# Optimization experiments

Measured on AMD Instinct MI355X. Metric: run time of the kernel, lower is better.

Reference implementation:

```python
import jax, jax.numpy as jnp
import numpy as np

DIM = 256
HEADS = 4
HID = 64
GROUPS = 32
HHD = HEADS * HID  # 256
EPS = 1e-5


def group_norm(x, gamma, beta):
    # x: (B, C, H, W)
    B, C, H, W = x.shape
    xg = x.reshape(B, GROUPS, C // GROUPS, H, W)
    mean = xg.mean(axis=(2, 3, 4), keepdims=True)
    var = xg.var(axis=(2, 3, 4), keepdims=True)
    xg = (xg - mean) * jax.lax.rsqrt(var + EPS)
    xn = xg.reshape(B, C, H, W)
    return xn * gamma[None, :, None, None] + beta[None, :, None, None]


def conv1x1(x, w, b):
    # x: (B, Cin, H, W), w: (Cout, Cin), b: (Cout,)
    return jnp.einsum('bchw,oc->bohw', x, w) + b[None, :, None, None]


def setup_inputs() -> dict:
    key = jax.random.key(0)
    ks = jax.random.split(key, 9)
    x = jax.random.normal(ks[0], (64, DIM, 32, 32), dtype=jnp.float32)
    s_in = 1.0 / np.sqrt(DIM)
    s_out = 1.0 / np.sqrt(HHD)
    wq = jax.random.uniform(ks[1], (HHD, DIM), jnp.float32, -s_in, s_in)
    bq = jax.random.uniform(ks[2], (HHD,), jnp.float32, -s_in, s_in)
    wk = jax.random.uniform(ks[3], (HHD, DIM), jnp.float32, -s_in, s_in)
    bk = jax.random.uniform(ks[4], (HHD,), jnp.float32, -s_in, s_in)
    wv = jax.random.uniform(ks[5], (HHD, DIM), jnp.float32, -s_in, s_in)
    bv = jax.random.uniform(ks[6], (HHD,), jnp.float32, -s_in, s_in)
    wo = jax.random.uniform(ks[7], (DIM, HHD), jnp.float32, -s_out, s_out)
    bo = jax.random.uniform(ks[8], (DIM,), jnp.float32, -s_out, s_out)
    gamma = jnp.ones((DIM,), jnp.float32)
    beta = jnp.zeros((DIM,), jnp.float32)
    return {"x": x, "wq": wq, "bq": bq, "wk": wk, "bk": bk, "wv": wv,
            "bv": bv, "wo": wo, "bo": bo, "gamma": gamma, "beta": beta}


def reference(x, wq, bq, wk, bk, wv, bv, wo, bo, gamma, beta):
    B, C, H, W = x.shape
    xn = group_norm(x, gamma, beta)  # residual uses normalized x (as in source)
    q = conv1x1(xn, wq, bq)  # (B, HHD, H, W)
    k = conv1x1(xn, wk, bk)
    v = conv1x1(xn, wv, bv)
    hw = H * W
    q = q.transpose(0, 2, 3, 1).reshape(B, hw, HHD)   # (B, HW, C)
    k = k.reshape(B, HHD, hw)                          # (B, C, HW)
    v = v.transpose(0, 2, 3, 1).reshape(B, hw, HHD)
    scale = 1.0 / np.sqrt(HID)  # source scales by sqrt(hidden_dimension) only
    qk = jnp.einsum('bnc,bcm->bnm', q, k) * scale      # (B, HW, HW)
    attn = jax.nn.softmax(qk, axis=-1)
    out = jnp.einsum('bnm,bmc->bnc', attn, v)          # (B, HW, HHD)
    out = out.reshape(B, H, W, HHD).transpose(0, 3, 1, 2)
    out = conv1x1(out, wo, bo)                         # (B, DIM, H, W)
    return xn + out
```

## Files before the change

### kernel.cpp

```cpp
#include <hip/hip_runtime.h>
#include <hip/hip_bf16.h>

typedef __attribute__((ext_vector_type(8))) short short8;
typedef __attribute__((ext_vector_type(4))) float f32x4;
typedef __attribute__((ext_vector_type(4))) unsigned short us4;

#define MFMA16(a,b,c) __builtin_amdgcn_mfma_f32_16x16x32_bf16((a),(b),(c),0,0,0)

__device__ __forceinline__ unsigned short f2bf(float x){
  union{float f; unsigned u;} v; v.f=x;
  unsigned r = v.u + 0x7fffu + ((v.u>>16)&1u);
  return (unsigned short)(r>>16);
}
__device__ __forceinline__ float bf2f(unsigned short u){
  union{unsigned u; float f;} v; v.u = ((unsigned)u)<<16; return v.f;
}

__global__ __launch_bounds__(256) void prep_kernel(
    const float* __restrict__ wq, const float* __restrict__ wk,
    const float* __restrict__ wv, const float* __restrict__ wo,
    unsigned short* __restrict__ dst){
  int idx = (blockIdx.x*256 + threadIdx.x)*4;
  const float* srcs[4] = {wq, wk, wv, wo};
  int m = idx >> 16;
  float4 v = *(const float4*)(srcs[m] + (idx & 65535));
  us4 o; o[0]=f2bf(v.x); o[1]=f2bf(v.y); o[2]=f2bf(v.z); o[3]=f2bf(v.w);
  *(us4*)(dst + idx) = o;
}

__global__ __launch_bounds__(256) void gn_kernel(
    const float* __restrict__ x, const float* __restrict__ gamma,
    const float* __restrict__ beta,
    unsigned short* __restrict__ xn_cm, unsigned short* __restrict__ xn_pm){
  int b = blockIdx.x >> 5, g = blockIdx.x & 31;
  int t = threadIdx.x;
  const float* xb = x + (size_t)(b*256 + g*8)*1024;
  float4 v[8]; float s=0.f, ss=0.f;
  #pragma unroll
  for(int j=0;j<8;++j){
    v[j] = ((const float4*)xb)[j*256 + t];
    s  += v[j].x+v[j].y+v[j].z+v[j].w;
    ss += v[j].x*v[j].x+v[j].y*v[j].y+v[j].z*v[j].z+v[j].w*v[j].w;
  }
  #pragma unroll
  for(int m=1;m<64;m<<=1){ s += __shfl_xor(s,m); ss += __shfl_xor(ss,m); }
  __shared__ float red[8];
  if((t&63)==0){ red[t>>6]=s; red[4+(t>>6)]=ss; }
  __syncthreads();
  s  = red[0]+red[1]+red[2]+red[3];
  ss = red[4]+red[5]+red[6]+red[7];
  float mean = s*(1.f/8192.f);
  float rstd = rsqrtf(ss*(1.f/8192.f) - mean*mean + 1e-5f);
  float fn[8][4];
  #pragma unroll
  for(int j=0;j<8;++j){
    float ga = gamma[g*8+j]*rstd;
    float be = beta[g*8+j] - mean*ga;
    fn[j][0]=v[j].x*ga+be; fn[j][1]=v[j].y*ga+be;
    fn[j][2]=v[j].z*ga+be; fn[j][3]=v[j].w*ga+be;
    us4 o; o[0]=f2bf(fn[j][0]); o[1]=f2bf(fn[j][1]);
          o[2]=f2bf(fn[j][2]); o[3]=f2bf(fn[j][3]);
    *(us4*)(xn_cm + (size_t)(b*256 + g*8 + j)*1024 + 4*t) = o;
  }
  #pragma unroll
  for(int pp=0;pp<4;++pp){
    short8 w8;
    #pragma unroll
    for(int j=0;j<8;++j) w8[j] = (short)f2bf(fn[j][pp]);
    *(short8*)(xn_pm + (size_t)(b*1024 + 4*t + pp)*256 + g*8) = w8;
  }
}

__global__ __launch_bounds__(256) void qkv_kernel(
    const unsigned short* __restrict__ xn_pm, const unsigned short* __restrict__ wbf,
    const float* __restrict__ bq, const float* __restrict__ bk,
    const float* __restrict__ bv,
    unsigned short* __restrict__ qb, unsigned short* __restrict__ kb,
    unsigned short* __restrict__ vTb){
  int b = blockIdx.y, z = blockIdx.z;
  int otile = blockIdx.x & 3, ptile = blockIdx.x >> 2;
  int t = threadIdx.x, w = t>>6, lane = t&63, lo = lane&15, hi = lane>>4;
  const unsigned short* W = wbf + (size_t)z*65536;
  const float* bias = (z==0)? bq : ((z==1)? bk : bv);
  const unsigned short* xb = xn_pm + (size_t)b*1024*256;
  int p0 = ptile*256 + w*64;
  f32x4 acc[4][4] = {};
  if(z < 2){
    #pragma unroll
    for(int kk=0;kk<8;++kk){
      short8 af[4], bfr[4];
      #pragma unroll
      for(int r=0;r<4;++r)
        af[r] = *(const short8*)(W + (size_t)(otile*64 + r*16 + lo)*256 + kk*32 + hi*8);
      #pragma unroll
      for(int c=0;c<4;++c)
        bfr[c] = *(const short8*)(xb + (size_t)(p0 + c*16 + lo)*256 + kk*32 + hi*8);
      #pragma unroll
      for(int r=0;r<4;++r)
        #pragma unroll
        for(int c=0;c<4;++c) acc[r][c] = MFMA16(af[r], bfr[c], acc[r][c]);
    }
    unsigned short* dst = (z==0)? qb : kb;
    float scale = (z==0)? 0.125f : 1.0f;
    #pragma unroll
    for(int r=0;r<4;++r){
      int ob = otile*64 + r*16 + hi*4;
      float4 bi = *(const float4*)(bias + ob);
      float bia[4] = {bi.x, bi.y, bi.z, bi.w};
      #pragma unroll
      for(int c=0;c<4;++c){
        int p = p0 + c*16 + lo;
        us4 stv;
        #pragma unroll
        for(int rg=0; rg<4; ++rg) stv[rg] = f2bf((acc[r][c][rg] + bia[rg])*scale);
        *(us4*)(dst + (size_t)(b*1024 + p)*256 + ob) = stv;
      }
    }
  } else {
    #pragma unroll
    for(int kk=0;kk<8;++kk){
      short8 af[4], bfr[4];
      #pragma unroll
      for(int r=0;r<4;++r)
        af[r] = *(const short8*)(xb + (size_t)(p0 + r*16 + lo)*256 + kk*32 + hi*8);
      #pragma unroll
      for(int c=0;c<4;++c)
        bfr[c] = *(const short8*)(W + (size_t)(otile*64 + c*16 + lo)*256 + kk*32 + hi*8);
      #pragma unroll
      for(int r=0;r<4;++r)
        #pragma unroll
        for(int c=0;c<4;++c) acc[r][c] = MFMA16(af[r], bfr[c], acc[r][c]);
    }
    #pragma unroll
    for(int c=0;c<4;++c){
      int o = otile*64 + c*16 + lo;
      float bia = bias[o];
      #pragma unroll
      for(int r=0;r<4;++r){
        int pb = p0 + r*16 + hi*4;
        us4 stv;
        #pragma unroll
        for(int rg=0; rg<4; ++rg) stv[rg] = f2bf(acc[r][c][rg] + bia);
        *(us4*)(vTb + (size_t)b*262144 + (size_t)o*1024 + pb) = stv;
      }
    }
  }
}

__global__ __launch_bounds__(256) void attn_kernel(
    const unsigned short* __restrict__ qb, const unsigned short* __restrict__ kb,
    const unsigned short* __restrict__ vT, const unsigned short* __restrict__ wo_bf,
    const float* __restrict__ bo, const unsigned short* __restrict__ xn_cm,
    float* __restrict__ out){
  int qt = blockIdx.x, b = blockIdx.y;
  int t = threadIdx.x, w = t>>6, lane = t&63, lo = lane&15, hi = lane>>4;
  __shared__ unsigned short smem_u[21248];
  unsigned short* k_lds = smem_u;
  unsigned short* v_lds = smem_u + 8448;
  unsigned short* p_lds = smem_u + 18688 + w*640;
  unsigned short* o_lds = smem_u + w*4224;

  short8 aq[8];
  const unsigned short* qrow = qb + (size_t)(b*1024 + qt*64 + w*16 + lo)*256;
  #pragma unroll
  for(int kk=0;kk<8;++kk) aq[kk] = *(const short8*)(qrow + kk*32 + hi*8);

  f32x4 oc[16] = {};
  float mr[4] = {-1e30f,-1e30f,-1e30f,-1e30f};
  float lr[4] = {0.f,0.f,0.f,0.f};

  const unsigned short* kbase = kb + (size_t)b*1024*256;
  const unsigned short* vbase = vT + (size_t)b*256*1024;

  for(int kv0=0; kv0<1024; kv0+=32){
    __syncthreads();
    {
      const short8* src = (const short8*)(kbase + (size_t)kv0*256);
      #pragma unroll
      for(int i=0;i<4;++i){
        int u = i*256 + t;
        *(short8*)(k_lds + (u>>5)*264 + (u&31)*8) = src[u];
      }
      #pragma unroll
      for(int i=0;i<4;++i){
        int u = i*256 + t;
        int c = u>>2, part = u&3;
        *(short8*)(v_lds + c*40 + part*8) =
            *(const short8*)(vbase + (size_t)c*1024 + kv0 + part*8);
      }
    }
    __syncthreads();
    f32x4 sc[2] = {};
    #pragma unroll
    for(int kk=0;kk<8;++kk){
      short8 b0 = *(const short8*)(k_lds + lo*264      + kk*32 + hi*8);
      short8 b1 = *(const short8*)(k_lds + (16+lo)*264 + kk*32 + hi*8);
      sc[0] = MFMA16(aq[kk], b0, sc[0]);
      sc[1] = MFMA16(aq[kk], b1, sc[1]);
    }
    float pr[2][4];
    #pragma unroll
    for(int r=0;r<4;++r){
      float tm = fmaxf(sc[0][r], sc[1][r]);
      tm = fmaxf(tm, __shfl_xor(tm,1)); tm = fmaxf(tm, __shfl_xor(tm,2));
      tm = fmaxf(tm, __shfl_xor(tm,4)); tm = fmaxf(tm, __shfl_xor(tm,8));
      float mnew  = fmaxf(mr[r], tm);
      float alpha = __expf(mr[r]-mnew);
      mr[r] = mnew;
      float p0v = __expf(sc[0][r]-mnew);
      float p1v = __expf(sc[1][r]-mnew);
      pr[0][r]=p0v; pr[1][r]=p1v;
      float rs = p0v + p1v;
      rs += __shfl_xor(rs,1); rs += __shfl_xor(rs,2);
      rs += __shfl_xor(rs,4); rs += __shfl_xor(rs,8);
      lr[r] = lr[r]*alpha + rs;
      #pragma unroll
      for(int f=0; f<16; ++f) oc[f][r] *= alpha;
    }
    #pragma unroll
    for(int cf=0;cf<2;++cf)
      #pragma unroll
      for(int r=0;r<4;++r)
        p_lds[(hi*4+r)*40 + cf*16 + lo] = f2bf(pr[cf][r]);
    short8 pa = *(const short8*)(p_lds + lo*40 + hi*8);
    #pragma unroll
    for(int f=0; f<16; ++f){
      short8 bv = *(const short8*)(v_lds + (f*16+lo)*40 + hi*8);
      oc[f] = MFMA16(pa, bv, oc[f]);
    }
  }

  float inv[4];
  #pragma unroll
  for(int r=0;r<4;++r) inv[r] = 1.f/lr[r];
  __syncthreads();
  #pragma unroll
  for(int f=0;f<16;++f)
    #pragma unroll
    for(int r=0;r<4;++r)
      o_lds[(hi*4+r)*264 + f*16 + lo] = f2bf(oc[f][r]*inv[r]);

  f32x4 a2[16] = {};
  #pragma unroll
  for(int kk=0;kk<8;++kk){
    short8 pa2 = *(const short8*)(o_lds + lo*264 + kk*32 + hi*8);
    #pragma unroll
    for(int cf=0;cf<16;++cf){
      short8 wb = *(const short8*)(wo_bf + (size_t)(cf*16+lo)*256 + kk*32 + hi*8);
      a2[cf] = MFMA16(pa2, wb, a2[cf]);
    }
  }
  int p0 = qt*64 + w*16 + hi*4;
  #pragma unroll
  for(int cf=0;cf<16;++cf){
    int o = cf*16 + lo;
    float bia = bo[o];
    us4 xr = *(const us4*)(xn_cm + (size_t)(b*256+o)*1024 + p0);
    float4 st;
    st.x = a2[cf][0] + bia + bf2f(xr[0]);
    st.y = a2[cf][1] + bia + bf2f(xr[1]);
    st.z = a2[cf][2] + bia + bf2f(xr[2]);
    st.w = a2[cf][3] + bia + bf2f(xr[3]);
    *(float4*)(out + (size_t)(b*256+o)*1024 + p0) = st;
  }
}

extern "C" void kernel_launch(void* const* d_in, const int* in_sizes, int n_in,
                              void* d_out, int out_size, void* d_ws, size_t ws_size,
                              hipStream_t stream){
  (void)in_sizes; (void)n_in; (void)out_size; (void)ws_size;
  const float* x     = (const float*)d_in[0];
  const float* wq    = (const float*)d_in[1];
  const float* bq    = (const float*)d_in[2];
  const float* wk    = (const float*)d_in[3];
  const float* bk    = (const float*)d_in[4];
  const float* wv    = (const float*)d_in[5];
  const float* bv    = (const float*)d_in[6];
  const float* wo    = (const float*)d_in[7];
  const float* bo    = (const float*)d_in[8];
  const float* gamma = (const float*)d_in[9];
  const float* beta  = (const float*)d_in[10];
  float* out = (float*)d_out;
  char* ws = (char*)d_ws;
  unsigned short* xn_cm = (unsigned short*)(ws);
  unsigned short* xn_pm = (unsigned short*)(ws + 33554432);
  unsigned short* qb    = (unsigned short*)(ws + 67108864);
  unsigned short* kb    = (unsigned short*)(ws + 100663296);
  unsigned short* vT    = (unsigned short*)(ws + 134217728);
  unsigned short* wbf   = (unsigned short*)(ws + 167772160);

  hipLaunchKernelGGL(prep_kernel, dim3(256), dim3(256), 0, stream, wq, wk, wv, wo, wbf);
  hipLaunchKernelGGL(gn_kernel,   dim3(2048), dim3(256), 0, stream, x, gamma, beta, xn_cm, xn_pm);
  hipLaunchKernelGGL(qkv_kernel,  dim3(16,64,3), dim3(256), 0, stream,
                     xn_pm, wbf, bq, bk, bv, qb, kb, vT);
  hipLaunchKernelGGL(attn_kernel, dim3(16,64), dim3(256), 0, stream,
                     qb, kb, vT, wbf + 3*65536, bo, xn_cm, out);
}
```

Baseline: 613.4 us.

## Double-buffer K/V via global_load_lds with swizzled LDS and lazy softmax rescale

```diff
diff --git a/kernel.cpp b/kernel.cpp
--- a/kernel.cpp
+++ b/kernel.cpp
@@ -6,6 +6,9 @@
 typedef __attribute__((ext_vector_type(4))) unsigned short us4;
 
 #define MFMA16(a,b,c) __builtin_amdgcn_mfma_f32_16x16x32_bf16((a),(b),(c),0,0,0)
+#define GLOAD16(g,l) __builtin_amdgcn_global_load_lds( \
+    (const __attribute__((address_space(1))) void*)(g), \
+    (__attribute__((address_space(3))) void*)(l), 16, 0, 0)
 
 __device__ __forceinline__ unsigned short f2bf(float x){
   union{float f; unsigned u;} v; v.f=x;
@@ -147,93 +150,126 @@
   }
 }
 
-__global__ __launch_bounds__(256) void attn_kernel(
+__global__ __launch_bounds__(512, 4) void attn_kernel(
     const unsigned short* __restrict__ qb, const unsigned short* __restrict__ kb,
     const unsigned short* __restrict__ vT, const unsigned short* __restrict__ wo_bf,
     const float* __restrict__ bo, const unsigned short* __restrict__ xn_cm,
     float* __restrict__ out){
-  int qt = blockIdx.x, b = blockIdx.y;
+  int flat = blockIdx.x;
+  int xcd = flat & 7, rest = flat >> 3;
+  int b = xcd*8 + (rest>>3), qt = rest & 7;
   int t = threadIdx.x, w = t>>6, lane = t&63, lo = lane&15, hi = lane>>4;
-  __shared__ unsigned short smem_u[21248];
-  unsigned short* k_lds = smem_u;
-  unsigned short* v_lds = smem_u + 8448;
-  unsigned short* p_lds = smem_u + 18688 + w*640;
-  unsigned short* o_lds = smem_u + w*4224;
+
+  __shared__ unsigned short smem_u[37888];
+  unsigned short* kb0 = smem_u;
+  unsigned short* kb1 = smem_u + 8192;
+  unsigned short* vb0 = smem_u + 16384;
+  unsigned short* vb1 = smem_u + 24576;
+  unsigned short* p_lds = smem_u + 32768 + w*640;
+
+  const unsigned short* kbase = kb + (size_t)b*262144;
+  const unsigned short* vbase = vT + (size_t)b*262144;
+
+  int ku0 = w*128 + lane, ku1 = w*128 + 64 + lane;
+  int kr0 = ku0>>5, kr1 = ku1>>5;
+  int ksrc0 = kr0*256 + ((ku0&31)^(kr0&7))*8;
+  int ksrc1 = kr1*256 + ((ku1&31)^(kr1&7))*8;
+  int vc0 = ku0>>2, vc1 = ku1>>2;
+  int vsrc0 = vc0*1024 + ((ku0&3)^(vc0&3))*8;
+  int vsrc1 = vc1*1024 + ((ku1&3)^(vc1&3))*8;
+  int ldsA = (w*128)*8, ldsB = (w*128+64)*8;
+
+  int hxl8 = (hi ^ (lo&7))*8;
+  int vroff = lo*32 + (hi^(lo&3))*8;
 
   short8 aq[8];
-  const unsigned short* qrow = qb + (size_t)(b*1024 + qt*64 + w*16 + lo)*256;
-  #pragma unroll
-  for(int kk=0;kk<8;++kk) aq[kk] = *(const short8*)(qrow + kk*32 + hi*8);
-
+  {
+    const unsigned short* qrow = qb + (size_t)(b*1024 + qt*128 + w*16 + lo)*256 + hi*8;
+    #pragma unroll
+    for(int kk=0;kk<8;++kk) aq[kk] = *(const short8*)(qrow + kk*32);
+  }
   f32x4 oc[16] = {};
   float mr[4] = {-1e30f,-1e30f,-1e30f,-1e30f};
   float lr[4] = {0.f,0.f,0.f,0.f};
 
-  const unsigned short* kbase = kb + (size_t)b*1024*256;
-  const unsigned short* vbase = vT + (size_t)b*256*1024;
-
-  for(int kv0=0; kv0<1024; kv0+=32){
+  {
+    const unsigned short* kg = kbase;
+    const unsigned short* vg = vbase;
+    GLOAD16(kg + ksrc0, kb0 + 0 + ldsA);  GLOAD16(kg + ksrc1, kb0 + 0 + ldsB);
+    GLOAD16(vg + vsrc0, vb0 + 0 + ldsA);  GLOAD16(vg + vsrc1, vb0 + 0 + ldsB);
+  }
+  __syncthreads();
+
+  for(int tkv=0; tkv<32; ++tkv){
+    int cur = tkv & 1;
+    unsigned short* kc = cur ? kb1 : kb0;
+    unsigned short* vc = cur ? vb1 : vb0;
+    if(tkv < 31){
+      unsigned short* kn = cur ? kb0 : kb1;
+      unsigned short* vn = cur ? vb0 : vb1;
+      const unsigned short* kg = kbase + (tkv+1)*32*256;
+      const unsigned short* vg = vbase + (tkv+1)*32;
+      GLOAD16(kg + ksrc0, kn + ldsA);  GLOAD16(kg + ksrc1, kn + ldsB);
+      GLOAD16(vg + vsrc0, vn + ldsA);  GLOAD16(vg + vsrc1, vn + ldsB);
+    }
+    f32x4 sc0 = {}, sc1 = {};
+    __builtin_amdgcn_s_setprio(1);
+    #pragma unroll
+    for(int kk=0;kk<8;++kk){
+      int coff = (kk*32) ^ hxl8;
+      short8 b0 = *(const short8*)(kc + lo*256        + coff);
+      short8 b1 = *(const short8*)(kc + lo*256 + 4096 + coff);
+      sc0 = MFMA16(aq[kk], b0, sc0);
+      sc1 = MFMA16(aq[kk], b1, sc1);
+    }
+    __builtin_amdgcn_s_setprio(0);
+    float tm[4];
+    #pragma unroll
+    for(int r=0;r<4;++r){
+      float m2 = fmaxf(sc0[r], sc1[r]);
+      m2 = fmaxf(m2, __shfl_xor(m2,1)); m2 = fmaxf(m2, __shfl_xor(m2,2));
+      m2 = fmaxf(m2, __shfl_xor(m2,4)); m2 = fmaxf(m2, __shfl_xor(m2,8));
+      tm[r] = m2;
+    }
+    if(__any((tm[0]>mr[0]+8.f)|(tm[1]>mr[1]+8.f)|(tm[2]>mr[2]+8.f)|(tm[3]>mr[3]+8.f))){
+      #pragma unroll
+      for(int r=0;r<4;++r){
+        float mnew  = fmaxf(mr[r], tm[r]);
+        float alpha = __expf(mr[r]-mnew);
+        mr[r] = mnew; lr[r] *= alpha;
+        #pragma unroll
+        for(int f=0; f<16; ++f) oc[f][r] *= alpha;
+      }
+    }
+    #pragma unroll
+    for(int r=0;r<4;++r){
+      float p0 = __expf(sc0[r]-mr[r]);
+      float p1 = __expf(sc1[r]-mr[r]);
+      lr[r] += p0 + p1;
+      p_lds[(hi*4+r)*40 + lo]    = f2bf(p0);
+      p_lds[(hi*4+r)*40 + 16+lo] = f2bf(p1);
+    }
+    short8 pa = *(const short8*)(p_lds + lo*40 + hi*8);
+    __builtin_amdgcn_s_setprio(1);
+    #pragma unroll
+    for(int f=0; f<16; ++f){
+      short8 bv = *(const short8*)(vc + f*512 + vroff);
+      oc[f] = MFMA16(pa, bv, oc[f]);
+    }
+    __builtin_amdgcn_s_setprio(0);
     __syncthreads();
-    {
-      const short8* src = (const short8*)(kbase + (size_t)kv0*256);
-      #pragma unroll
-      for(int i=0;i<4;++i){
-        int u = i*256 + t;
-        *(short8*)(k_lds + (u>>5)*264 + (u&31)*8) = src[u];
-      }
-      #pragma unroll
-      for(int i=0;i<4;++i){
-        int u = i*256 + t;
-        int c = u>>2, part = u&3;
-        *(short8*)(v_lds + c*40 + part*8) =
-            *(const short8*)(vbase + (size_t)c*1024 + kv0 + part*8);
-      }
-    }
-    __syncthreads();
-    f32x4 sc[2] = {};
-    #pragma unroll
-    for(int kk=0;kk<8;++kk){
-      short8 b0 = *(const short8*)(k_lds + lo*264      + kk*32 + hi*8);
-      short8 b1 = *(const short8*)(k_lds + (16+lo)*264 + kk*32 + hi*8);
-      sc[0] = MFMA16(aq[kk], b0, sc[0]);
-      sc[1] = MFMA16(aq[kk], b1, sc[1]);
-    }
-    float pr[2][4];
-    #pragma unroll
-    for(int r=0;r<4;++r){
-      float tm = fmaxf(sc[0][r], sc[1][r]);
-      tm = fmaxf(tm, __shfl_xor(tm,1)); tm = fmaxf(tm, __shfl_xor(tm,2));
-      tm = fmaxf(tm, __shfl_xor(tm,4)); tm = fmaxf(tm, __shfl_xor(tm,8));
-      float mnew  = fmaxf(mr[r], tm);
-      float alpha = __expf(mr[r]-mnew);
-      mr[r] = mnew;
-      float p0v = __expf(sc[0][r]-mnew);
-      float p1v = __expf(sc[1][r]-mnew);
-      pr[0][r]=p0v; pr[1][r]=p1v;
-      float rs = p0v + p1v;
-      rs += __shfl_xor(rs,1); rs += __shfl_xor(rs,2);
-      rs += __shfl_xor(rs,4); rs += __shfl_xor(rs,8);
-      lr[r] = lr[r]*alpha + rs;
-      #pragma unroll
-      for(int f=0; f<16; ++f) oc[f][r] *= alpha;
-    }
-    #pragma unroll
-    for(int cf=0;cf<2;++cf)
-      #pragma unroll
-      for(int r=0;r<4;++r)
-        p_lds[(hi*4+r)*40 + cf*16 + lo] = f2bf(pr[cf][r]);
-    short8 pa = *(const short8*)(p_lds + lo*40 + hi*8);
-    #pragma unroll
-    for(int f=0; f<16; ++f){
-      short8 bv = *(const short8*)(v_lds + (f*16+lo)*40 + hi*8);
-      oc[f] = MFMA16(pa, bv, oc[f]);
-    }
-  }
-
+  }
+
+  #pragma unroll
+  for(int r=0;r<4;++r){
+    lr[r] += __shfl_xor(lr[r],1); lr[r] += __shfl_xor(lr[r],2);
+    lr[r] += __shfl_xor(lr[r],4); lr[r] += __shfl_xor(lr[r],8);
+  }
   float inv[4];
   #pragma unroll
   for(int r=0;r<4;++r) inv[r] = 1.f/lr[r];
-  __syncthreads();
+
+  unsigned short* o_lds = smem_u + w*4224;
   #pragma unroll
   for(int f=0;f<16;++f)
     #pragma unroll
@@ -250,18 +286,18 @@
       a2[cf] = MFMA16(pa2, wb, a2[cf]);
     }
   }
-  int p0 = qt*64 + w*16 + hi*4;
+  int p0r = qt*128 + w*16 + hi*4;
   #pragma unroll
   for(int cf=0;cf<16;++cf){
     int o = cf*16 + lo;
     float bia = bo[o];
-    us4 xr = *(const us4*)(xn_cm + (size_t)(b*256+o)*1024 + p0);
+    us4 xr = *(const us4*)(xn_cm + (size_t)(b*256+o)*1024 + p0r);
     float4 st;
     st.x = a2[cf][0] + bia + bf2f(xr[0]);
     st.y = a2[cf][1] + bia + bf2f(xr[1]);
     st.z = a2[cf][2] + bia + bf2f(xr[2]);
     st.w = a2[cf][3] + bia + bf2f(xr[3]);
-    *(float4*)(out + (size_t)(b*256+o)*1024 + p0) = st;
+    *(float4*)(out + (size_t)(b*256+o)*1024 + p0r) = st;
   }
 }
 
@@ -293,6 +329,6 @@
   hipLaunchKernelGGL(gn_kernel,   dim3(2048), dim3(256), 0, stream, x, gamma, beta, xn_cm, xn_pm);
   hipLaunchKernelGGL(qkv_kernel,  dim3(16,64,3), dim3(256), 0, stream,
                      xn_pm, wbf, bq, bk, bv, qb, kb, vT);
-  hipLaunchKernelGGL(attn_kernel, dim3(16,64), dim3(256), 0, stream,
+  hipLaunchKernelGGL(attn_kernel, dim3(512), dim3(512), 0, stream,
                      qb, kb, vT, wbf + 3*65536, bo, xn_cm, out);
 }
```

Measured after the change: 543.8 us. 1.13x faster.
